# Performance work log

Measured on AMD Instinct MI355X. Metric: run time of the kernel, lower is better.

The kernel has to match this reference:

```python
import jax, jax.numpy as jnp
import numpy as np

N_NODES = 50000
N_EDGES = 800000
C_IN = 128
C_OUT = 256
BN_EPS = 1e-5


def setup_inputs() -> dict:
    key = jax.random.key(0)
    k1, k2, k3, k4, k5 = jax.random.split(key, 5)
    x = jax.random.normal(k1, (N_NODES, C_IN), dtype=jnp.float32)
    src = jax.random.randint(k2, (N_EDGES,), 0, N_NODES, dtype=jnp.int64)
    dst = jax.random.randint(k3, (N_EDGES,), 0, N_NODES, dtype=jnp.int64)
    theta_w = jax.random.normal(k4, (C_OUT, C_IN), dtype=jnp.float32) * 0.05
    phi_w = jax.random.normal(k5, (C_OUT, C_IN), dtype=jnp.float32) * 0.05
    gamma = jnp.ones((C_OUT,), dtype=jnp.float32)
    beta = jnp.zeros((C_OUT,), dtype=jnp.float32)
    return {"x": x, "src": src, "dst": dst, "theta_w": theta_w,
            "phi_w": phi_w, "gamma": gamma, "beta": beta}


def reference(x, src, dst, theta_w, phi_w, gamma, beta):
    # gather endpoint features: xi = x[src], xj = x[dst]
    xi = x[src]                      # [E, c_in]
    xj = x[dst]                      # [E, c_in]
    # e_ij = relu(theta(xj - xi) + phi(xi))  -> [E, c_out]
    e = jax.nn.relu((xj - xi) @ theta_w.T + xi @ phi_w.T)
    # scatter-max aggregate per source node; empty segments -> 0 (matches
    # torch.scatter_reduce amax with include_self=False leaving zeros)
    n = x.shape[0]
    agg = jax.ops.segment_max(e, src, num_segments=n)  # [N, c_out]
    agg = jnp.where(jnp.isneginf(agg), jnp.zeros((), agg.dtype), agg)
    # BatchNorm1d (training mode: batch statistics, biased variance)
    mean = jnp.mean(agg, axis=0)
    var = jnp.var(agg, axis=0)
    y = (agg - mean) * jax.lax.rsqrt(var + BN_EPS) * gamma + beta
    return jax.nn.relu(y)
```

## Files before the change

kernel.cpp:

```cpp
#include <hip/hip_runtime.h>

#define N_NODES 50000
#define N_EDGES 800000
#define C_IN 128
#define C_OUT 256
#define BN_EPS 1e-5f
#define SL 8
#define SLC 32
#define NPB 128
#define PAD 8
#define CAP 48

#define HB 782
#define GBX ((N_NODES + 127) / 128)
#define GB (GBX * 8)

using short8  = __attribute__((ext_vector_type(8))) short;
using floatx4 = __attribute__((ext_vector_type(4))) float;
using h2      = __attribute__((ext_vector_type(2))) _Float16;

union UH2 { unsigned int u; h2 h; };
union HS  { _Float16 f; unsigned short s; };

__device__ __forceinline__ h2 pkmax(h2 a, h2 b) {
    return __builtin_elementwise_max(a, b);
}

__device__ __forceinline__ unsigned short f2bf(float f) {
    unsigned int u = __float_as_uint(f);
    u = (u + 0x7fffu + ((u >> 16) & 1u)) >> 16;
    return (unsigned short)u;
}

#define XQ (N_NODES * C_IN / 4)
#define WQ (512 * C_IN / 4)

__global__ __launch_bounds__(256) void prep(
    const float* __restrict__ x, const float* __restrict__ theta,
    const float* __restrict__ phi, const int* __restrict__ src,
    const int* __restrict__ dst,
    unsigned short* __restrict__ xb, unsigned short* __restrict__ wb,
    int* __restrict__ deg, unsigned short* __restrict__ edst2)
{
    const int tid = threadIdx.x;
    if (blockIdx.x < HB) {
        const int base = blockIdx.x * 1024 + tid;
        #pragma unroll
        for (int k = 0; k < 4; ++k) {
            int e = base + k * 256;
            if (e < N_EDGES) {
                int s = src[e];
                int d = dst[e];
                int r = atomicAdd(&deg[s], 1);
                if (r < CAP)
                    edst2[s * CAP + r] = (unsigned short)d;
            }
        }
        return;
    }
    int i = (blockIdx.x - HB) * 256 + tid;
    if (i < XQ) {
        float4 vv = ((const float4*)x)[i];
        ((ushort4*)xb)[i] = make_ushort4(f2bf(vv.x), f2bf(vv.y),
                                         f2bf(vv.z), f2bf(vv.w));
    } else if (i < XQ + WQ) {
        int j = i - XQ;
        float4 t;
        if (j < 256 * C_IN / 4) {
            t = ((const float4*)theta)[j];
        } else {
            int k = j - 256 * C_IN / 4;
            float4 th = ((const float4*)theta)[k];
            float4 ph = ((const float4*)phi)[k];
            t = make_float4(ph.x - th.x, ph.y - th.y, ph.z - th.z, ph.w - th.w);
        }
        ((ushort4*)wb)[j] = make_ushort4(f2bf(t.x), f2bf(t.y),
                                         f2bf(t.z), f2bf(t.w));
    }
}

__global__ __launch_bounds__(256) void gemm(
    const unsigned short* __restrict__ xb,
    const unsigned short* __restrict__ wb,
    unsigned short* __restrict__ u,
    unsigned short* __restrict__ v)
{
    __shared__ unsigned short Bs[64][C_IN + PAD];
    const int tid = threadIdx.x;

    const int b = blockIdx.x;
    const int bx = b >> 3;
    const int by = b & 7;
    const int wave = tid >> 6;
    const int lane = tid & 63;
    const int l15 = lane & 15;
    const int quad = lane >> 4;

    {
        int r = tid >> 2;
        int q = tid & 3;
        const uint4* sp = (const uint4*)(wb + (size_t)(by * 64 + r) * C_IN + q * 32);
        #pragma unroll
        for (int i = 0; i < 4; ++i) *(uint4*)&Bs[r][q * 32 + i * 8] = sp[i];
    }

    const int n0 = bx * 128 + wave * 32 + l15;
    const unsigned short* arow0 = xb + (size_t)min(n0,      N_NODES - 1) * C_IN + quad * 8;
    const unsigned short* arow1 = xb + (size_t)min(n0 + 16, N_NODES - 1) * C_IN + quad * 8;

    __syncthreads();

    floatx4 acc[2][4];
    #pragma unroll
    for (int mi = 0; mi < 2; ++mi)
        #pragma unroll
        for (int ni = 0; ni < 4; ++ni)
            acc[mi][ni] = (floatx4){0.f, 0.f, 0.f, 0.f};

    #pragma unroll
    for (int ks = 0; ks < 4; ++ks) {
        short8 a[2], bfr[4];
        a[0] = *(const short8*)(arow0 + ks * 32);
        a[1] = *(const short8*)(arow1 + ks * 32);
        #pragma unroll
        for (int ni = 0; ni < 4; ++ni)
            bfr[ni] = *(const short8*)&Bs[ni * 16 + l15][ks * 32 + quad * 8];
        #pragma unroll
        for (int mi = 0; mi < 2; ++mi)
            #pragma unroll
            for (int ni = 0; ni < 4; ++ni)
                acc[mi][ni] = __builtin_amdgcn_mfma_f32_16x16x32_bf16(
                    bfr[ni], a[mi], acc[mi][ni], 0, 0, 0);
    }

    const bool is_u = (by < 4);
    unsigned short* dstbuf = is_u ? u : v;
    #pragma unroll
    for (int mi = 0; mi < 2; ++mi) {
        const int n = bx * 128 + wave * 32 + mi * 16 + l15;
        if (n >= N_NODES) continue;
        #pragma unroll
        for (int ni = 0; ni < 4; ++ni) {
            const int cb = by * 64 + ni * 16 + quad * 4;
            const int s = (cb >> 5) & 7;
            const int o = cb & 31;
            HS h0, h1, h2_, h3;
            h0.f = (_Float16)acc[mi][ni][0];
            h1.f = (_Float16)acc[mi][ni][1];
            h2_.f = (_Float16)acc[mi][ni][2];
            h3.f = (_Float16)acc[mi][ni][3];
            *(ushort4*)(dstbuf + ((size_t)s * N_NODES + n) * SLC + o) =
                make_ushort4(h0.s, h1.s, h2_.s, h3.s);
        }
    }
}

__global__ __launch_bounds__(256) void gather_slice(
    const int* __restrict__ deg, const unsigned short* __restrict__ edst2,
    const unsigned short* __restrict__ u, unsigned short* __restrict__ v,
    float* __restrict__ sums, float* __restrict__ sumsq)
{
    __shared__ unsigned short elds[NPB * CAP];
    __shared__ int degs[NPB];
    __shared__ float red[16][16][4];

    const int slice = blockIdx.x & 7;
    const int chunk = blockIdx.x >> 3;
    const int tid = threadIdx.x;
    const int g16 = tid >> 4;
    const int l16 = tid & 15;
    const int es  = l16 >> 2;
    const int c4  = l16 & 3;
    const int c16 = c4 * 16;
    const int cp  = c4 * 8 + es * 2;

    const int cn = chunk * NPB;

    if (tid < NPB) {
        int n = cn + tid;
        degs[tid] = (n < N_NODES) ? deg[n] : 0;
    }
    {
        const uint4* gsrc = (const uint4*)(edst2 + (size_t)cn * CAP);
        #pragma unroll
        for (int t = tid; t < NPB * CAP / 8; t += 256)
            ((uint4*)elds)[t] = gsrc[t];
    }
    __syncthreads();

    const char* ub = (const char*)(u + (size_t)slice * N_NODES * SLC);
    unsigned short* vb = v + (size_t)slice * N_NODES * SLC;

    float s1_0 = 0.f, s1_1 = 0.f, s2_0 = 0.f, s2_1 = 0.f;

    #pragma unroll 1
    for (int i = 0; i < NPB / 16; ++i) {
        const int nl = i * 16 + g16;
        const int n = cn + nl;
        if (n >= N_NODES) continue;
        const int d = degs[nl];

        unsigned int* vp = (unsigned int*)(vb + (size_t)n * SLC + cp);
        UH2 wv; wv.u = *vp;

        UH2 m0, m1, m2, m3;
        m0.u = m1.u = m2.u = m3.u = 0xFC00FC00u;

        const int base = nl * CAP;
        const int nit = (d + 15) >> 4;
        const int lim = base + d - 1;
        int b16 = base + es;
        for (int r = 0; r < nit; ++r, b16 += 16) {
            int i0 = min(b16,      lim);
            int i1 = min(b16 + 4,  lim);
            int i2 = min(b16 + 8,  lim);
            int i3 = min(b16 + 12, lim);
            int d0 = elds[i0];
            int d1 = elds[i1];
            int d2 = elds[i2];
            int d3 = elds[i3];
            uint4 w0 = *(const uint4*)(ub + ((d0 << 6) | c16));
            uint4 w1 = *(const uint4*)(ub + ((d1 << 6) | c16));
            uint4 w2 = *(const uint4*)(ub + ((d2 << 6) | c16));
            uint4 w3 = *(const uint4*)(ub + ((d3 << 6) | c16));
            UH2 a_, b_, c_, e_;
            a_.u = w0.x; b_.u = w1.x; c_.u = w2.x; e_.u = w3.x;
            m0.h = pkmax(m0.h, pkmax(pkmax(a_.h, b_.h), pkmax(c_.h, e_.h)));
            a_.u = w0.y; b_.u = w1.y; c_.u = w2.y; e_.u = w3.y;
            m1.h = pkmax(m1.h, pkmax(pkmax(a_.h, b_.h), pkmax(c_.h, e_.h)));
            a_.u = w0.z; b_.u = w1.z; c_.u = w2.z; e_.u = w3.z;
            m2.h = pkmax(m2.h, pkmax(pkmax(a_.h, b_.h), pkmax(c_.h, e_.h)));
            a_.u = w0.w; b_.u = w1.w; c_.u = w2.w; e_.u = w3.w;
            m3.h = pkmax(m3.h, pkmax(pkmax(a_.h, b_.h), pkmax(c_.h, e_.h)));
        }

        UH2 t;
        t.u = (unsigned)__shfl_xor((int)m0.u, 4); m0.h = pkmax(m0.h, t.h);
        t.u = (unsigned)__shfl_xor((int)m1.u, 4); m1.h = pkmax(m1.h, t.h);
        t.u = (unsigned)__shfl_xor((int)m2.u, 4); m2.h = pkmax(m2.h, t.h);
        t.u = (unsigned)__shfl_xor((int)m3.u, 4); m3.h = pkmax(m3.h, t.h);
        t.u = (unsigned)__shfl_xor((int)m0.u, 8); m0.h = pkmax(m0.h, t.h);
        t.u = (unsigned)__shfl_xor((int)m1.u, 8); m1.h = pkmax(m1.h, t.h);
        t.u = (unsigned)__shfl_xor((int)m2.u, 8); m2.h = pkmax(m2.h, t.h);
        t.u = (unsigned)__shfl_xor((int)m3.u, 8); m3.h = pkmax(m3.h, t.h);

        UH2 s01, s23, mm;
        s01.u = (es & 1) ? m1.u : m0.u;
        s23.u = (es & 1) ? m3.u : m2.u;
        mm.u  = (es & 2) ? s23.u : s01.u;

        float a0 = fmaxf((float)wv.h[0] + (float)mm.h[0], 0.f);
        float a1 = fmaxf((float)wv.h[1] + (float)mm.h[1], 0.f);

        UH2 pw;
        pw.h[0] = (_Float16)a0;
        pw.h[1] = (_Float16)a1;
        *vp = pw.u;

        s1_0 += a0; s1_1 += a1;
        s2_0 += a0 * a0; s2_1 += a1 * a1;
    }

    __syncthreads();
    red[g16][l16][0] = s1_0; red[g16][l16][1] = s1_1;
    red[g16][l16][2] = s2_0; red[g16][l16][3] = s2_1;
    __syncthreads();
    if (tid < 16) {
        const int tt = tid;
        float r0 = 0.f, r1 = 0.f, r2 = 0.f, r3 = 0.f;
        #pragma unroll
        for (int g = 0; g < 16; ++g) {
            r0 += red[g][tt][0]; r1 += red[g][tt][1];
            r2 += red[g][tt][2]; r3 += red[g][tt][3];
        }
        const int c = slice * SLC + ((tt & 3) * 8 + (tt >> 2) * 2);
        atomicAdd(&sums[c + 0], r0);
        atomicAdd(&sums[c + 1], r1);
        atomicAdd(&sumsq[c + 0], r2);
        atomicAdd(&sumsq[c + 1], r3);
    }
}

__global__ __launch_bounds__(256) void bn_apply(
    const unsigned short* __restrict__ agg,
    float* __restrict__ out, const float* __restrict__ sums,
    const float* __restrict__ sumsq, const float* __restrict__ gamma,
    const float* __restrict__ beta)
{
    __shared__ float cA[C_OUT], cB[C_OUT];
    const int tid = threadIdx.x;
    {
        const float inv_n = 1.f / (float)N_NODES;
        const float mean = sums[tid] * inv_n;
        const float var = sumsq[tid] * inv_n - mean * mean;
        const float s = rsqrtf(var + BN_EPS) * gamma[tid];
        cA[tid] = s;
        cB[tid] = beta[tid] - mean * s;
    }
    __syncthreads();

    const size_t base = (size_t)blockIdx.x * 2048 + (size_t)tid * 8;
    const int slice  = (int)(base / ((size_t)N_NODES * SLC));
    const int within = (int)(base % ((size_t)N_NODES * SLC));
    const int n  = within >> 5;
    const int c  = slice * SLC + (within & 31);

    uint4 w = *(const uint4*)(agg + base);
    const float4 A0 = *(const float4*)(cA + c);
    const float4 A1 = *(const float4*)(cA + c + 4);
    const float4 B0 = *(const float4*)(cB + c);
    const float4 B1 = *(const float4*)(cB + c + 4);

    UH2 t;
    float4 o0, o1;
    t.u = w.x;
    o0.x = fmaxf((float)t.h[0] * A0.x + B0.x, 0.f);
    o0.y = fmaxf((float)t.h[1] * A0.y + B0.y, 0.f);
    t.u = w.y;
    o0.z = fmaxf((float)t.h[0] * A0.z + B0.z, 0.f);
    o0.w = fmaxf((float)t.h[1] * A0.w + B0.w, 0.f);
    t.u = w.z;
    o1.x = fmaxf((float)t.h[0] * A1.x + B1.x, 0.f);
    o1.y = fmaxf((float)t.h[1] * A1.y + B1.y, 0.f);
    t.u = w.w;
    o1.z = fmaxf((float)t.h[0] * A1.z + B1.z, 0.f);
    o1.w = fmaxf((float)t.h[1] * A1.w + B1.w, 0.f);

    float* op = out + (size_t)n * C_OUT + c;
    *(float4*)op = o0;
    *(float4*)(op + 4) = o1;
}

extern "C" void kernel_launch(void* const* d_in, const int* in_sizes, int n_in,
                              void* d_out, int out_size, void* d_ws, size_t ws_size,
                              hipStream_t stream) {
    const float* x     = (const float*)d_in[0];
    const int*   src   = (const int*)d_in[1];
    const int*   dst   = (const int*)d_in[2];
    const float* theta = (const float*)d_in[3];
    const float* phi   = (const float*)d_in[4];
    const float* gamma = (const float*)d_in[5];
    const float* beta  = (const float*)d_in[6];
    float* out = (float*)d_out;

    char* ws = (char*)d_ws;
    const size_t uv_elems = (size_t)N_NODES * C_OUT;
    unsigned short* u = (unsigned short*)ws;
    unsigned short* v = u + uv_elems;
    float* sums   = (float*)(v + uv_elems);
    float* sumsq  = sums + C_OUT;
    int*   deg    = (int*)(sumsq + C_OUT);
    unsigned short* edst2 = (unsigned short*)(deg + N_NODES);
    unsigned short* xb = edst2 + (size_t)(N_NODES + NPB) * CAP;
    unsigned short* wb = xb + (size_t)N_NODES * C_IN;

    hipMemsetAsync(sums, 0, (2 * C_OUT + N_NODES) * sizeof(int), stream);

    prep<<<HB + (XQ + WQ + 255) / 256, 256, 0, stream>>>(
        x, theta, phi, src, dst, xb, wb, deg, edst2);

    gemm<<<GB, 256, 0, stream>>>(xb, wb, u, v);

    const int chunks = (N_NODES + NPB - 1) / NPB;
    gather_slice<<<chunks * SL, 256, 0, stream>>>(
        deg, edst2, u, v, sums, sumsq);

    bn_apply<<<(int)(((size_t)N_NODES * C_OUT) / 2048), 256, 0, stream>>>(
        v, out, sums, sumsq, gamma, beta);
}
```

Baseline: 230.2 us.

## Replace global-atomic edge bucketing with two-level radix partition via LDS histograms

Edge bucketing used to run one global atomicAdd per edge on per-node degree counters. It now does a coarse histogram on src>>8 in shared memory, an exclusive scan per bucket across blocks, and a scatter of packed (low src, dst) words into a bucket-ordered buffer. A final pass, folded into the GEMM launch as extra blocks, builds per-node adjacency with shared-memory atomics. The aim is to remove contended global atomics and scattered writes, at the cost of two more kernel launches and extra passes over the edge arrays. The output buffer is reused as scratch space, and the per-node order of dst entries differs, which the later max reduction does not depend on.

```diff
diff --git a/kernel.cpp b/kernel.cpp
--- a/kernel.cpp
+++ b/kernel.cpp
@@ -10,6 +10,7 @@
 #define NPB 128
 #define PAD 8
 #define CAP 48
+#define NHI 196
 
 #define HB 782
 #define GBX ((N_NODES + 127) / 128)
@@ -35,27 +36,33 @@
 #define XQ (N_NODES * C_IN / 4)
 #define WQ (512 * C_IN / 4)
 
-__global__ __launch_bounds__(256) void prep(
+__global__ __launch_bounds__(256) void count_convert(
     const float* __restrict__ x, const float* __restrict__ theta,
     const float* __restrict__ phi, const int* __restrict__ src,
-    const int* __restrict__ dst,
     unsigned short* __restrict__ xb, unsigned short* __restrict__ wb,
-    int* __restrict__ deg, unsigned short* __restrict__ edst2)
-{
+    int* __restrict__ counts_t)
+{
+    __shared__ int hist[NHI];
     const int tid = threadIdx.x;
     if (blockIdx.x < HB) {
-        const int base = blockIdx.x * 1024 + tid;
-        #pragma unroll
-        for (int k = 0; k < 4; ++k) {
-            int e = base + k * 256;
-            if (e < N_EDGES) {
-                int s = src[e];
-                int d = dst[e];
-                int r = atomicAdd(&deg[s], 1);
-                if (r < CAP)
-                    edst2[s * CAP + r] = (unsigned short)d;
+        for (int t = tid; t < NHI; t += 256) hist[t] = 0;
+        __syncthreads();
+        const int e0 = blockIdx.x * 1024 + tid * 4;
+        if (e0 + 3 < N_EDGES) {
+            int4 s4 = *(const int4*)(src + e0);
+            atomicAdd(&hist[s4.x >> 8], 1);
+            atomicAdd(&hist[s4.y >> 8], 1);
+            atomicAdd(&hist[s4.z >> 8], 1);
+            atomicAdd(&hist[s4.w >> 8], 1);
+        } else {
+            for (int k = 0; k < 4; ++k) {
+                int e = e0 + k;
+                if (e < N_EDGES) atomicAdd(&hist[src[e] >> 8], 1);
             }
         }
+        __syncthreads();
+        for (int t = tid; t < NHI; t += 256)
+            counts_t[t * HB + blockIdx.x] = hist[t];
         return;
     }
     int i = (blockIdx.x - HB) * 256 + tid;
@@ -79,16 +86,124 @@
     }
 }
 
-__global__ __launch_bounds__(256) void gemm(
+__global__ __launch_bounds__(1024) void scan_counts(
+    const int* __restrict__ counts_t, int* __restrict__ offs_t,
+    int* __restrict__ totals)
+{
+    __shared__ int s[1024];
+    const int h = blockIdx.x;
+    const int tid = threadIdx.x;
+    int own = (tid < HB) ? counts_t[h * HB + tid] : 0;
+    s[tid] = own;
+    __syncthreads();
+    for (int d = 1; d < 1024; d <<= 1) {
+        int t = (tid >= d) ? s[tid - d] : 0;
+        __syncthreads();
+        s[tid] += t;
+        __syncthreads();
+    }
+    if (tid < HB) offs_t[h * HB + tid] = s[tid] - own;
+    if (tid == 1023) totals[h] = s[1023];
+}
+
+__global__ __launch_bounds__(256) void scatter_hi(
+    const int* __restrict__ src, const int* __restrict__ dst,
+    const int* __restrict__ offs_t, const int* __restrict__ totals,
+    unsigned int* __restrict__ ebuf)
+{
+    __shared__ int cnt[NHI];
+    __shared__ int obl[NHI];
+    __shared__ int bas[256];
+    const int tid = threadIdx.x;
+    const int blk = blockIdx.x;
+
+    int tv = (tid < NHI) ? totals[tid] : 0;
+    bas[tid] = tv;
+    __syncthreads();
+    for (int d = 1; d < 256; d <<= 1) {
+        int t = (tid >= d) ? bas[tid - d] : 0;
+        __syncthreads();
+        bas[tid] += t;
+        __syncthreads();
+    }
+    int excl = bas[tid] - tv;
+    __syncthreads();
+    bas[tid] = excl;
+    if (tid < NHI) {
+        cnt[tid] = 0;
+        obl[tid] = offs_t[tid * HB + blk];
+    }
+    __syncthreads();
+
+    const int e0 = blk * 1024 + tid * 4;
+    if (e0 + 3 < N_EDGES) {
+        int4 s4 = *(const int4*)(src + e0);
+        int4 d4 = *(const int4*)(dst + e0);
+        int h0 = s4.x >> 8, h1 = s4.y >> 8, h2 = s4.z >> 8, h3 = s4.w >> 8;
+        int l0 = atomicAdd(&cnt[h0], 1);
+        int l1 = atomicAdd(&cnt[h1], 1);
+        int l2 = atomicAdd(&cnt[h2], 1);
+        int l3 = atomicAdd(&cnt[h3], 1);
+        ebuf[bas[h0] + obl[h0] + l0] = (unsigned)(s4.x & 255) | ((unsigned)d4.x << 8);
+        ebuf[bas[h1] + obl[h1] + l1] = (unsigned)(s4.y & 255) | ((unsigned)d4.y << 8);
+        ebuf[bas[h2] + obl[h2] + l2] = (unsigned)(s4.z & 255) | ((unsigned)d4.z << 8);
+        ebuf[bas[h3] + obl[h3] + l3] = (unsigned)(s4.w & 255) | ((unsigned)d4.w << 8);
+    } else {
+        for (int k = 0; k < 4; ++k) {
+            int e = e0 + k;
+            if (e < N_EDGES) {
+                int s_ = src[e], d_ = dst[e];
+                int hh = s_ >> 8;
+                int l = atomicAdd(&cnt[hh], 1);
+                ebuf[bas[hh] + obl[hh] + l] = (unsigned)(s_ & 255) | ((unsigned)d_ << 8);
+            }
+        }
+    }
+}
+
+__global__ __launch_bounds__(256) void fin_gemm(
     const unsigned short* __restrict__ xb,
     const unsigned short* __restrict__ wb,
     unsigned short* __restrict__ u,
-    unsigned short* __restrict__ v)
+    unsigned short* __restrict__ v,
+    const int* __restrict__ totals, const unsigned int* __restrict__ ebuf,
+    int* __restrict__ deg, unsigned short* __restrict__ edst2)
 {
     __shared__ unsigned short Bs[64][C_IN + PAD];
     const int tid = threadIdx.x;
 
-    const int b = blockIdx.x;
+    if (blockIdx.x < NHI) {
+        int* cnt2 = (int*)&Bs[0][0];
+        int* sc   = cnt2 + 256;
+        const int h = blockIdx.x;
+        int tv = (tid < NHI) ? totals[tid] : 0;
+        sc[tid] = tv;
+        cnt2[tid] = 0;
+        __syncthreads();
+        for (int d = 1; d < 256; d <<= 1) {
+            int t = (tid >= d) ? sc[tid - d] : 0;
+            __syncthreads();
+            sc[tid] += t;
+            __syncthreads();
+        }
+        const int s1 = sc[h];
+        const int cnth = totals[h];
+        const int s0 = s1 - cnth;
+        for (int i = s0 + tid; i < s1; i += 256) {
+            unsigned w = ebuf[i];
+            int nl = (int)(w & 255u);
+            int d_ = (int)(w >> 8);
+            int r = atomicAdd(&cnt2[nl], 1);
+            if (r < CAP)
+                edst2[(size_t)((h << 8) + nl) * CAP + r] = (unsigned short)d_;
+        }
+        __syncthreads();
+        int n = (h << 8) + tid;
+        if (n < N_NODES) deg[n] = cnt2[tid];
+        return;
+    }
+
+    const int b = blockIdx.x - NHI;
     const int bx = b >> 3;
     const int by = b & 7;
     const int wave = tid >> 6;
@@ -354,12 +469,22 @@
     unsigned short* xb = edst2 + (size_t)(N_NODES + NPB) * CAP;
     unsigned short* wb = xb + (size_t)N_NODES * C_IN;
 
-    hipMemsetAsync(sums, 0, (2 * C_OUT + N_NODES) * sizeof(int), stream);
-
-    prep<<<HB + (XQ + WQ + 255) / 256, 256, 0, stream>>>(
-        x, theta, phi, src, dst, xb, wb, deg, edst2);
-
-    gemm<<<GB, 256, 0, stream>>>(xb, wb, u, v);
+    unsigned int* ebuf  = (unsigned int*)out;
+    int* counts_t       = (int*)(out + 1000000);
+    int* offs_t         = (int*)(out + 1200000);
+    int* totals         = (int*)(out + 1400000);
+
+    hipMemsetAsync(sums, 0, 2 * C_OUT * sizeof(float), stream);
+
+    count_convert<<<HB + (XQ + WQ + 255) / 256, 256, 0, stream>>>(
+        x, theta, phi, src, xb, wb, counts_t);
+
+    scan_counts<<<NHI, 1024, 0, stream>>>(counts_t, offs_t, totals);
+
+    scatter_hi<<<HB, 256, 0, stream>>>(src, dst, offs_t, totals, ebuf);
+
+    fin_gemm<<<NHI + GB, 256, 0, stream>>>(
+        xb, wb, u, v, totals, ebuf, deg, edst2);
 
     const int chunks = (N_NODES + NPB - 1) / NPB;
     gather_slice<<<chunks * SL, 256, 0, stream>>>(
```

Measured after the change: 204.0 us. -11.4%, faster.

## Replace global per-node atomics with two-pass bucketed edge CSR build

Applied to the files above, without the earlier changes.

Edge bucketing now runs in two passes. A shared-memory histogram by src>>8 reserves ranges in 196 global buckets, and packed (local src, dst) words go into a staging buffer that reuses the output array. A second pass, fused into the GEMM launch as extra blocks, builds the per-node adjacency lists using shared-memory atomics and writes deg directly, which also shrinks the memset. The aim is to remove contended global atomics and scattered global writes on deg. The cost is an extra read and write of the staging buffer and a dependence on a bucket capacity (4608) that could drop edges in a skewed bucket.

```diff
diff --git a/kernel.cpp b/kernel.cpp
--- a/kernel.cpp
+++ b/kernel.cpp
@@ -10,6 +10,8 @@
 #define NPB 128
 #define PAD 8
 #define CAP 48
+#define NHI 196
+#define EBCAP 4608
 
 #define HB 782
 #define GBX ((N_NODES + 127) / 128)
@@ -35,29 +37,67 @@
 #define XQ (N_NODES * C_IN / 4)
 #define WQ (512 * C_IN / 4)
 
-__global__ __launch_bounds__(256) void prep(
+__global__ __launch_bounds__(256) void bucket_convert(
     const float* __restrict__ x, const float* __restrict__ theta,
     const float* __restrict__ phi, const int* __restrict__ src,
     const int* __restrict__ dst,
     unsigned short* __restrict__ xb, unsigned short* __restrict__ wb,
-    int* __restrict__ deg, unsigned short* __restrict__ edst2)
+    int* __restrict__ gcur, unsigned int* __restrict__ ebuf)
 {
+    __shared__ int hist[NHI];
+    __shared__ int basg[NHI];
+    __shared__ int cur[NHI];
     const int tid = threadIdx.x;
+
     if (blockIdx.x < HB) {
-        const int base = blockIdx.x * 1024 + tid;
+        for (int t = tid; t < NHI; t += 256) { hist[t] = 0; cur[t] = 0; }
+        __syncthreads();
+
+        const int e0 = blockIdx.x * 1024 + tid * 4;
+        int4 s4, d4;
+        bool full = (e0 + 3 < N_EDGES);
+        if (full) {
+            s4 = *(const int4*)(src + e0);
+            d4 = *(const int4*)(dst + e0);
+            atomicAdd(&hist[s4.x >> 8], 1);
+            atomicAdd(&hist[s4.y >> 8], 1);
+            atomicAdd(&hist[s4.z >> 8], 1);
+            atomicAdd(&hist[s4.w >> 8], 1);
+        } else {
+            s4 = make_int4(0, 0, 0, 0); d4 = s4;
+            for (int k = 0; k < 4; ++k) {
+                int e = e0 + k;
+                if (e < N_EDGES) {
+                    int sv = src[e], dv = dst[e];
+                    ((int*)&s4)[k] = sv; ((int*)&d4)[k] = dv;
+                    atomicAdd(&hist[sv >> 8], 1);
+                }
+            }
+        }
+        __syncthreads();
+
+        if (tid < NHI) {
+            int c = hist[tid];
+            basg[tid] = c ? atomicAdd(&gcur[tid], c) : 0;
+        }
+        __syncthreads();
+
         #pragma unroll
         for (int k = 0; k < 4; ++k) {
-            int e = base + k * 256;
+            int e = e0 + k;
             if (e < N_EDGES) {
-                int s = src[e];
-                int d = dst[e];
-                int r = atomicAdd(&deg[s], 1);
-                if (r < CAP)
-                    edst2[s * CAP + r] = (unsigned short)d;
+                int sv = ((int*)&s4)[k], dv = ((int*)&d4)[k];
+                int hh = sv >> 8;
+                int l = atomicAdd(&cur[hh], 1);
+                int pos = basg[hh] + l;
+                if (pos < EBCAP)
+                    ebuf[hh * EBCAP + pos] =
+                        (unsigned)(sv & 255) | ((unsigned)dv << 8);
             }
         }
         return;
     }
+
     int i = (blockIdx.x - HB) * 256 + tid;
     if (i < XQ) {
         float4 vv = ((const float4*)x)[i];
@@ -79,16 +119,39 @@
     }
 }
 
-__global__ __launch_bounds__(256) void gemm(
+__global__ __launch_bounds__(256) void fin_gemm(
     const unsigned short* __restrict__ xb,
     const unsigned short* __restrict__ wb,
     unsigned short* __restrict__ u,
-    unsigned short* __restrict__ v)
+    unsigned short* __restrict__ v,
+    const int* __restrict__ gcur, const unsigned int* __restrict__ ebuf,
+    int* __restrict__ deg, unsigned short* __restrict__ edst2)
 {
     __shared__ unsigned short Bs[64][C_IN + PAD];
     const int tid = threadIdx.x;
 
-    const int b = blockIdx.x;
+    if (blockIdx.x < NHI) {
+        int* cnt2 = (int*)&Bs[0][0];
+        const int h = blockIdx.x;
+        cnt2[tid] = 0;
+        __syncthreads();
+        const int total = min(gcur[h], EBCAP);
+        const int s0 = h * EBCAP;
+        for (int i = s0 + tid; i < s0 + total; i += 256) {
+            unsigned w = ebuf[i];
+            int nl = (int)(w & 255u);
+            int d_ = (int)(w >> 8);
+            int r = atomicAdd(&cnt2[nl], 1);
+            if (r < CAP)
+                edst2[(size_t)((h << 8) + nl) * CAP + r] = (unsigned short)d_;
+        }
+        __syncthreads();
+        int n = (h << 8) + tid;
+        if (n < N_NODES) deg[n] = cnt2[tid];
+        return;
+    }
+
+    const int b = blockIdx.x - NHI;
     const int bx = b >> 3;
     const int by = b & 7;
     const int wave = tid >> 6;
@@ -349,17 +412,21 @@
     unsigned short* v = u + uv_elems;
     float* sums   = (float*)(v + uv_elems);
     float* sumsq  = sums + C_OUT;
-    int*   deg    = (int*)(sumsq + C_OUT);
+    int*   gcur   = (int*)(sumsq + C_OUT);
+    int*   deg    = gcur + NHI + 4;
     unsigned short* edst2 = (unsigned short*)(deg + N_NODES);
     unsigned short* xb = edst2 + (size_t)(N_NODES + NPB) * CAP;
     unsigned short* wb = xb + (size_t)N_NODES * C_IN;
 
-    hipMemsetAsync(sums, 0, (2 * C_OUT + N_NODES) * sizeof(int), stream);
-
-    prep<<<HB + (XQ + WQ + 255) / 256, 256, 0, stream>>>(
-        x, theta, phi, src, dst, xb, wb, deg, edst2);
-
-    gemm<<<GB, 256, 0, stream>>>(xb, wb, u, v);
+    unsigned int* ebuf = (unsigned int*)out;
+
+    hipMemsetAsync(sums, 0, (2 * C_OUT + NHI + 4) * sizeof(int), stream);
+
+    bucket_convert<<<HB + (XQ + WQ + 255) / 256, 256, 0, stream>>>(
+        x, theta, phi, src, dst, xb, wb, gcur, ebuf);
+
+    fin_gemm<<<NHI + GB, 256, 0, stream>>>(
+        xb, wb, u, v, gcur, ebuf, deg, edst2);
 
     const int chunks = (N_NODES + NPB - 1) / NPB;
     gather_slice<<<chunks * SL, 256, 0, stream>>>(
```

Result: faster. 206.1 us (-10.5%).
